# Performance work log

Measured on AMD Instinct MI355X. Metric: run time of the kernel, lower is better.

The kernel has to match this reference:

```python
import jax, jax.numpy as jnp
import numpy as np

BETA = 2
KERAS_EPS = 1e-7  # keras.backend.epsilon()


def _masks(n):
    idx = np.arange(n)
    # eps2[i,j] = 1 iff i<j  (itertools.combinations for N=2)
    eps2 = (idx[:, None] < idx[None, :]).astype(np.float32)
    # eps3[i,j,k] = 1 iff i<j<k  (itertools.combinations for N=3)
    eps3 = ((idx[:, None, None] < idx[None, :, None])
            & (idx[None, :, None] < idx[None, None, :])).astype(np.float32)
    return jnp.asarray(eps2), jnp.asarray(eps3)


def _jet_ecf(x, beta):
    # x: [B, n, 3] = (pt, eta, phi)
    n = x.shape[1]
    pt = x[:, :, 0]    # [B, n]
    eta = x[:, :, 1]
    phi = x[:, :, 2]
    # pairwise squared distance in (eta, phi): [B, n, n]
    R2 = (eta[:, :, None] - eta[:, None, :]) ** 2 \
       + (phi[:, :, None] - phi[:, None, :]) ** 2
    if beta == 2:
        Rb = R2
    elif beta == 1:
        Rb = jnp.sqrt(R2)
    else:
        Rb = R2 ** (beta / 2)

    eps2, eps3 = _masks(n)

    ecf1 = jnp.sum(pt, axis=-1, keepdims=True)                         # [B, 1]
    ecf2 = jnp.einsum('ij,ai,aj,aij->a', eps2, pt, pt, Rb)[:, None]    # [B, 1]
    ecf3 = jnp.einsum('ijk,ai,aj,ak,aij,aik,ajk->a',
                      eps3, pt, pt, pt, Rb, Rb, Rb)[:, None]           # [B, 1]
    return ecf1, ecf2, ecf3


def setup_inputs() -> dict:
    key = jax.random.key(0)
    x = jax.random.normal(key, (2048, 200, 3), dtype=jnp.float32)
    return {"x": x}


def reference(x):
    ecf1, ecf2, ecf3 = _jet_ecf(x, BETA)
    d2 = ecf3 * ecf1 ** 3 / (ecf2 ** 3 + KERAS_EPS)
    return jnp.concatenate([ecf1, ecf2, ecf3, d2], axis=-1)  # [B, 4]
```

## Files before the change

kernel.cpp:

```cpp
#include <hip/hip_runtime.h>


constexpr int NPART = 200;
constexpr int BLK = 256;

__global__ __launch_bounds__(BLK) void jet_ecf_kernel(const float* __restrict__ x,
                                                      float* __restrict__ out,
                                                      int njet) {
    __shared__ float s_pt[NPART], s_eta[NPART], s_phi[NPART];
    __shared__ float s_t[NPART];
    __shared__ double s_red[4][10];

    const int jet = blockIdx.x;
    if (jet >= njet) return;
    const int tid = threadIdx.x;
    const float* xj = x + (size_t)jet * NPART * 3;

    for (int p = tid; p < NPART; p += BLK) {
        s_pt[p]  = xj[p * 3 + 0];
        s_eta[p] = xj[p * 3 + 1];
        s_phi[p] = xj[p * 3 + 2];
    }
    __syncthreads();

    double acc[10];
    #pragma unroll
    for (int k = 0; k < 10; ++k) acc[k] = 0.0;
    for (int p = tid; p < NPART; p += BLK) {
        const double w = (double)s_pt[p];
        const double e = (double)s_eta[p];
        const double f = (double)s_phi[p];
        const double a = e * e + f * f;
        acc[0] += w;        acc[1] += w * a;     acc[2] += w * e;
        acc[3] += w * f;    acc[4] += w * a * a; acc[5] += w * a * e;
        acc[6] += w * a * f; acc[7] += w * e * e; acc[8] += w * f * f;
        acc[9] += w * e * f;
    }
    #pragma unroll
    for (int off = 32; off > 0; off >>= 1) {
        #pragma unroll
        for (int k = 0; k < 10; ++k) acc[k] += __shfl_down(acc[k], off, 64);
    }
    const int wid = tid >> 6, lane = tid & 63;
    if (lane == 0) {
        #pragma unroll
        for (int k = 0; k < 10; ++k) s_red[wid][k] = acc[k];
    }

    if (tid < NPART) {
        const float ej = s_eta[tid], pj = s_phi[tid];
        float s = 0.0f;
        for (int i = 0; i < tid; ++i) {
            const float de = __fsub_rn(s_eta[i], ej);
            const float dp = __fsub_rn(s_phi[i], pj);
            const float r2 = __fadd_rn(__fmul_rn(de, de), __fmul_rn(dp, dp));
            s = __fadd_rn(s, __fmul_rn(r2, s_pt[i]));
        }
        s_t[tid] = __fmul_rn(s_pt[tid], s);
    }
    __syncthreads();

    if (tid == 0) {
        float e2f = 0.0f;
        for (int j = 0; j < NPART; ++j) e2f = __fadd_rn(e2f, s_t[j]);

        double m[10];
        #pragma unroll
        for (int k = 0; k < 10; ++k)
            m[k] = s_red[0][k] + s_red[1][k] + s_red[2][k] + s_red[3][k];
        const double S = m[0], Sa = m[1], Se = m[2], Sp = m[3], Saa = m[4];
        const double Sae = m[5], Sap = m[6], See = m[7], Spp = m[8], Sep = m[9];

        const double A[4][4] = {
            {  Saa,        Sa,       -2.0 * Sae, -2.0 * Sap },
            {  Sa,         S,        -2.0 * Se,  -2.0 * Sp  },
            { -2.0 * Sae, -2.0 * Se,  4.0 * See,  4.0 * Sep },
            { -2.0 * Sap, -2.0 * Sp,  4.0 * Sep,  4.0 * Spp }
        };
        const double B[4][4] = {
            { Sa,  S,  -2.0 * Se,  -2.0 * Sp  },
            { Saa, Sa, -2.0 * Sae, -2.0 * Sap },
            { Sae, Se, -2.0 * See, -2.0 * Sep },
            { Sap, Sp, -2.0 * Sep, -2.0 * Spp }
        };
        const double C[4][4] = {
            { S,  Sa,  Se,  Sp  },
            { Sa, Saa, Sae, Sap },
            { Se, Sae, See, Sep },
            { Sp, Sap, Sep, Spp }
        };
        double T = 0.0;
        #pragma unroll
        for (int b = 0; b < 4; ++b) {
            #pragma unroll
            for (int g = 0; g < 4; ++g) {
                double ab = 0.0;
                #pragma unroll
                for (int al = 0; al < 4; ++al) ab += A[al][b] * B[al][g];
                T += ab * C[b][g];
            }
        }
        const double ecf1 = S;
        const double ecf2 = (double)e2f;
        const double ecf3 = T * (1.0 / 6.0);
        const double d2 = ecf3 * ecf1 * ecf1 * ecf1 / (ecf2 * ecf2 * ecf2 + 1e-7);
        float4 o = make_float4((float)ecf1, (float)ecf2, (float)ecf3, (float)d2);
        *reinterpret_cast<float4*>(out + (size_t)jet * 4) = o;
    }
}

extern "C" void kernel_launch(void* const* d_in, const int* in_sizes, int n_in,
                              void* d_out, int out_size, void* d_ws, size_t ws_size,
                              hipStream_t stream) {
    const float* x = (const float*)d_in[0];
    float* out = (float*)d_out;
    const int njet = in_sizes[0] / (NPART * 3);
    jet_ecf_kernel<<<njet, BLK, 0, stream>>>(x, out, njet);
}
```

Measured before the change: 76.70 us.

## Use single-wavefront blocks with register-resident particles and readlane broadcasts

```diff
diff --git a/kernel.cpp b/kernel.cpp
--- a/kernel.cpp
+++ b/kernel.cpp
@@ -2,75 +2,130 @@
 
 
 constexpr int NPART = 200;
-constexpr int BLK = 256;
 
-__global__ __launch_bounds__(BLK) void jet_ecf_kernel(const float* __restrict__ x,
-                                                      float* __restrict__ out,
-                                                      int njet) {
-    __shared__ float s_pt[NPART], s_eta[NPART], s_phi[NPART];
-    __shared__ float s_t[NPART];
-    __shared__ double s_red[4][10];
+__device__ __forceinline__ float bcast(float v, int ii) {
+    return __int_as_float(__builtin_amdgcn_readlane(__float_as_int(v), ii));
+}
 
+__global__ __launch_bounds__(64) void jet_ecf_kernel(const float* __restrict__ x,
+                                                     float* __restrict__ out,
+                                                     int njet) {
     const int jet = blockIdx.x;
     if (jet >= njet) return;
-    const int tid = threadIdx.x;
+    const int lane = threadIdx.x;
     const float* xj = x + (size_t)jet * NPART * 3;
 
-    for (int p = tid; p < NPART; p += BLK) {
-        s_pt[p]  = xj[p * 3 + 0];
-        s_eta[p] = xj[p * 3 + 1];
-        s_phi[p] = xj[p * 3 + 2];
+    float pw[4], pe[4], pp[4];
+    #pragma unroll
+    for (int k = 0; k < 4; ++k) {
+        const int p = 64 * k + lane;
+        if (p < NPART) {
+            pw[k] = xj[p * 3 + 0];
+            pe[k] = xj[p * 3 + 1];
+            pp[k] = xj[p * 3 + 2];
+        } else {
+            pw[k] = 0.0f; pe[k] = 0.0f; pp[k] = 0.0f;
+        }
     }
-    __syncthreads();
 
-    double acc[10];
+    double S = 0, Sa = 0, Se = 0, Sp = 0, Saa = 0;
+    double Sae = 0, Sap = 0, See = 0, Spp = 0, Sep = 0;
     #pragma unroll
-    for (int k = 0; k < 10; ++k) acc[k] = 0.0;
-    for (int p = tid; p < NPART; p += BLK) {
-        const double w = (double)s_pt[p];
-        const double e = (double)s_eta[p];
-        const double f = (double)s_phi[p];
+    for (int k = 0; k < 4; ++k) {
+        const double w = (double)pw[k];
+        const double e = (double)pe[k];
+        const double f = (double)pp[k];
         const double a = e * e + f * f;
-        acc[0] += w;        acc[1] += w * a;     acc[2] += w * e;
-        acc[3] += w * f;    acc[4] += w * a * a; acc[5] += w * a * e;
-        acc[6] += w * a * f; acc[7] += w * e * e; acc[8] += w * f * f;
-        acc[9] += w * e * f;
+        S   += w;        Sa  += w * a;     Se  += w * e;
+        Sp  += w * f;    Saa += w * a * a; Sae += w * a * e;
+        Sap += w * a * f; See += w * e * e; Spp += w * f * f;
+        Sep += w * e * f;
     }
     #pragma unroll
     for (int off = 32; off > 0; off >>= 1) {
-        #pragma unroll
-        for (int k = 0; k < 10; ++k) acc[k] += __shfl_down(acc[k], off, 64);
-    }
-    const int wid = tid >> 6, lane = tid & 63;
-    if (lane == 0) {
-        #pragma unroll
-        for (int k = 0; k < 10; ++k) s_red[wid][k] = acc[k];
+        S   += __shfl_down(S,   off, 64);
+        Sa  += __shfl_down(Sa,  off, 64);
+        Se  += __shfl_down(Se,  off, 64);
+        Sp  += __shfl_down(Sp,  off, 64);
+        Saa += __shfl_down(Saa, off, 64);
+        Sae += __shfl_down(Sae, off, 64);
+        Sap += __shfl_down(Sap, off, 64);
+        See += __shfl_down(See, off, 64);
+        Spp += __shfl_down(Spp, off, 64);
+        Sep += __shfl_down(Sep, off, 64);
     }
 
-    if (tid < NPART) {
-        const float ej = s_eta[tid], pj = s_phi[tid];
-        float s = 0.0f;
-        for (int i = 0; i < tid; ++i) {
-            const float de = __fsub_rn(s_eta[i], ej);
-            const float dp = __fsub_rn(s_phi[i], pj);
-            const float r2 = __fadd_rn(__fmul_rn(de, de), __fmul_rn(dp, dp));
-            s = __fadd_rn(s, __fmul_rn(r2, s_pt[i]));
-        }
-        s_t[tid] = __fmul_rn(s_pt[tid], s);
+    float s0 = 0.0f, s1 = 0.0f, s2 = 0.0f, s3 = 0.0f;
+
+#define COL_BODY(ACC, K)                                                      \
+    {                                                                         \
+        const float de = __fsub_rn(ei, pe[K]);                                \
+        const float dp = __fsub_rn(pi, pp[K]);                                \
+        const float r2 = __fadd_rn(__fmul_rn(de, de), __fmul_rn(dp, dp));     \
+        ACC = __fadd_rn(ACC, __fmul_rn(r2, wi));                              \
     }
-    __syncthreads();
+#define COL_BODY_PRED(ACC, K)                                                 \
+    {                                                                         \
+        const float de = __fsub_rn(ei, pe[K]);                                \
+        const float dp = __fsub_rn(pi, pp[K]);                                \
+        const float r2 = __fadd_rn(__fmul_rn(de, de), __fmul_rn(dp, dp));     \
+        const float c  = __fmul_rn(r2, wi);                                   \
+        ACC = __fadd_rn(ACC, (ii < lane) ? c : 0.0f);                         \
+    }
 
-    if (tid == 0) {
-        float e2f = 0.0f;
-        for (int j = 0; j < NPART; ++j) e2f = __fadd_rn(e2f, s_t[j]);
+    #pragma unroll 4
+    for (int ii = 0; ii < 64; ++ii) {
+        const float ei = bcast(pe[0], ii);
+        const float pi = bcast(pp[0], ii);
+        const float wi = bcast(pw[0], ii);
+        COL_BODY_PRED(s0, 0)
+        COL_BODY(s1, 1)
+        COL_BODY(s2, 2)
+        COL_BODY(s3, 3)
+    }
+    #pragma unroll 4
+    for (int ii = 0; ii < 64; ++ii) {
+        const float ei = bcast(pe[1], ii);
+        const float pi = bcast(pp[1], ii);
+        const float wi = bcast(pw[1], ii);
+        COL_BODY_PRED(s1, 1)
+        COL_BODY(s2, 2)
+        COL_BODY(s3, 3)
+    }
+    #pragma unroll 4
+    for (int ii = 0; ii < 64; ++ii) {
+        const float ei = bcast(pe[2], ii);
+        const float pi = bcast(pp[2], ii);
+        const float wi = bcast(pw[2], ii);
+        COL_BODY_PRED(s2, 2)
+        COL_BODY(s3, 3)
+    }
+    #pragma unroll
+    for (int ii = 0; ii < 7; ++ii) {
+        const float ei = bcast(pe[3], ii);
+        const float pi = bcast(pp[3], ii);
+        const float wi = bcast(pw[3], ii);
+        COL_BODY_PRED(s3, 3)
+    }
+#undef COL_BODY
+#undef COL_BODY_PRED
 
-        double m[10];
-        #pragma unroll
-        for (int k = 0; k < 10; ++k)
-            m[k] = s_red[0][k] + s_red[1][k] + s_red[2][k] + s_red[3][k];
-        const double S = m[0], Sa = m[1], Se = m[2], Sp = m[3], Saa = m[4];
-        const double Sae = m[5], Sap = m[6], See = m[7], Spp = m[8], Sep = m[9];
+    const float t0 = __fmul_rn(pw[0], s0);
+    const float t1 = __fmul_rn(pw[1], s1);
+    const float t2 = __fmul_rn(pw[2], s2);
+    const float t3 = __fmul_rn(pw[3], s3);
 
+    float e2f = 0.0f;
+    #pragma unroll 8
+    for (int ii = 0; ii < 64; ++ii) e2f = __fadd_rn(e2f, bcast(t0, ii));
+    #pragma unroll 8
+    for (int ii = 0; ii < 64; ++ii) e2f = __fadd_rn(e2f, bcast(t1, ii));
+    #pragma unroll 8
+    for (int ii = 0; ii < 64; ++ii) e2f = __fadd_rn(e2f, bcast(t2, ii));
+    #pragma unroll
+    for (int ii = 0; ii < 8; ++ii)  e2f = __fadd_rn(e2f, bcast(t3, ii));
+
+    if (lane == 0) {
         const double A[4][4] = {
             {  Saa,        Sa,       -2.0 * Sae, -2.0 * Sap },
             {  Sa,         S,        -2.0 * Se,  -2.0 * Sp  },
@@ -115,5 +170,5 @@
     const float* x = (const float*)d_in[0];
     float* out = (float*)d_out;
     const int njet = in_sizes[0] / (NPART * 3);
-    jet_ecf_kernel<<<njet, BLK, 0, stream>>>(x, out, njet);
+    jet_ecf_kernel<<<njet, 64, 0, stream>>>(x, out, njet);
 }
```

Measured after the change: 74.19 us. -3.3%, faster.
